# Performance work log

Hardware: AMD Instinct MI355X
Metric: run time of the kernel (lower is better)

Reference implementation:

```python
import jax, jax.numpy as jnp
import numpy as np

GAMMA = 1.4
N_PTS, N_IC, HID = 32768, 16384, 128


def _mlp(layers, p):
    # tanh MLP; layers = list of (W, b), last layer linear
    h = p
    for W, b in layers[:-1]:
        h = jnp.tanh(h @ W + b)
    W, b = layers[-1]
    return h @ W + b


def setup_inputs() -> dict:
    key = jax.random.key(0)
    ks = jax.random.split(key, 16)
    d = {
        "x_train": jax.random.uniform(ks[0], (N_PTS, 3), jnp.float32),
        "x_initial": jax.random.uniform(ks[1], (N_IC, 3), jnp.float32),
        "ic": jax.random.uniform(ks[2], (4, 4), jnp.float32),
    }
    def lin(k, fi, fo):
        return jax.random.normal(k, (fi, fo), jnp.float32) * np.float32(np.sqrt(1.0 / fi))
    dims_m = [(3, HID), (HID, HID), (HID, HID), (HID, 4)]
    dims_n = [(3, HID), (HID, HID), (HID, HID), (HID, 1)]
    for i, (fi, fo) in enumerate(dims_m):
        d[f"mw{i}"] = lin(ks[3 + i], fi, fo)
        d[f"mb{i}"] = jnp.zeros((fo,), jnp.float32)
    for i, (fi, fo) in enumerate(dims_n):
        d[f"nw{i}"] = lin(ks[8 + i], fi, fo)
        d[f"nb{i}"] = jnp.zeros((fo,), jnp.float32)
    return d


def _loss(x_train, x_initial, ic,
          mw0, mb0, mw1, mb1, mw2, mb2, mw3, mb3,
          nw0, nb0, nw1, nb1, nw2, nb2, nw3, nb3):
    layers_m = [(mw0, mb0), (mw1, mb1), (mw2, mb2), (mw3, mb3)]
    layers_n = [(nw0, nb0), (nw1, nb1), (nw2, nb2), (nw3, nb3)]

    def prim(p):  # p: (3,) = (x, y, t)
        o = _mlp(layers_m, p)
        rho, pr, u, v = o[0], o[1], o[2], o[3]
        E = pr / (GAMMA - 1.0) + 0.5 * rho * (u * u + v * v)
        return rho, pr, u, v, E

    def Ufn(p):  # conserved state U1..U4
        rho, pr, u, v, E = prim(p)
        return jnp.stack([rho, rho * u, rho * v, E])

    def quant(p):  # [U1..U4, f1..f4, g1..g4]
        rho, pr, u, v, E = prim(p)
        U = jnp.stack([rho, rho * u, rho * v, E])
        f = jnp.stack([rho * u, rho * u * u + pr, rho * u * v, u * (E + pr)])
        g = jnp.stack([rho * v, rho * u * v, rho * v * v + pr, v * (E + pr)])
        return jnp.concatenate([U, f, g])

    # one fused forward-mode Jacobian sweep replaces 20 torch autograd.grad calls
    J = jax.vmap(jax.jacfwd(quant))(x_train)            # (N, 12, 3)
    Hs = jax.vmap(jax.jacfwd(jax.jacfwd(Ufn)))(x_train)  # (N, 4, 3, 3)

    mu = 0.01 * jnp.squeeze(_mlp(layers_n, x_train), -1) ** 2  # (N,)
    lap = Hs[:, :, 0, 0] + Hs[:, :, 1, 1]               # U_xx + U_yy, (N, 4)
    # res_i = U_i_t + f_i_x + g_i_y - mu * (U_i_xx + U_i_yy)
    res = J[:, 0:4, 2] + J[:, 4:8, 0] + J[:, 8:12, 1] - mu[:, None] * lap
    r = jnp.mean(res ** 2, axis=0)                      # (4,) -> r1..r4

    # initial-condition quadrant loss (masked means, jit-safe)
    pred = _mlp(layers_m, x_initial)                    # (Ni, 4)
    xl = x_initial[:, 0] < 0.5
    xr = x_initial[:, 0] > 0.5
    yt = x_initial[:, 1] > 0.5
    yb = x_initial[:, 1] < 0.5
    perm = jnp.array([0, 3, 1, 2])  # ic columns -> [rho, p, u, v] target order
    init_loss = jnp.float32(0.0)
    for row, mask in ((1, xl & yt), (3, xr & yt), (0, xl & yb), (2, xr & yb)):
        tgt = ic[row][perm]                             # (4,)
        m = mask.astype(pred.dtype)
        denom = jnp.maximum(jnp.sum(m), 1.0)
        init_loss = init_loss + jnp.sum(m[:, None] * (pred - tgt) ** 2) / denom

    return jnp.sum(r) + 10.0 * init_loss + 0.1 * jnp.mean(mu ** 2)


def reference(x_train, x_initial, ic,
              mw0, mb0, mw1, mb1, mw2, mb2, mw3, mb3,
              nw0, nb0, nw1, nb1, nw2, nb2, nw3, nb3):
    return _loss(x_train, x_initial, ic,
                 mw0, mb0, mw1, mb1, mw2, mb2, mw3, mb3,
                 nw0, nb0, nw1, nb1, nw2, nb2, nw3, nb3)
```

## Files before the change

kernel.cpp:

```cpp
#include <hip/hip_runtime.h>

#define NPTS 32768
#define NIC  16384
#define GRID 512
#define BLK  256
#define NW   4

typedef __attribute__((ext_vector_type(8))) _Float16 f16x8;
typedef __attribute__((ext_vector_type(4))) float f32x4;

#define SWZ(e, r) ((e) ^ (((r) & 7) << 3))
#define MFMA16 __builtin_amdgcn_mfma_f32_16x16x32_f16

__device__ __forceinline__ float tanh_fast(float x) {
    float e = __expf(2.0f * x);
    return 1.0f - 2.0f / (e + 1.0f);
}

__device__ __forceinline__ float wave_allsum(float v) {
#pragma unroll
    for (int off = 32; off > 0; off >>= 1) v += __shfl_xor(v, off, 64);
    return v;
}

__device__ __forceinline__ unsigned short f2hb(float x) {
    return __builtin_bit_cast(unsigned short, (_Float16)x);
}
__device__ __forceinline__ uint2 pack4h(float a, float b, float c, float d) {
    return make_uint2((unsigned)f2hb(a) | ((unsigned)f2hb(b) << 16),
                      (unsigned)f2hb(c) | ((unsigned)f2hb(d) << 16));
}

__global__ __launch_bounds__(512) void k_prep(
    const float* __restrict__ mw1, const float* __restrict__ mw2,
    const float* __restrict__ nw1, const float* __restrict__ nw2,
    const float* __restrict__ mw3,
    unsigned short* __restrict__ wt1, unsigned short* __restrict__ wt2,
    unsigned short* __restrict__ nt1, unsigned short* __restrict__ nt2,
    unsigned short* __restrict__ w3t) {
    const int tid = threadIdx.x;
    const int bk = blockIdx.x;
    if (bk == 4) {
        for (int i = tid; i < 2048; i += 512) w3t[i] = 0;
        __syncthreads();
        if (tid < 512) {
            const int j = tid & 127, k = tid >> 7;
            w3t[k * 128 + SWZ(j, k)] = f2hb(mw3[j * 4 + k]);
        }
        return;
    }
    const float* src = (bk == 0) ? mw1 : (bk == 1) ? mw2 : (bk == 2) ? nw1 : nw2;
    unsigned short* dst = (bk == 0) ? wt1 : (bk == 1) ? wt2 : (bk == 2) ? nt1 : nt2;
    __shared__ float sM[128 * 129];
#pragma unroll
    for (int k = 0; k < 32; k++) {
        const int idx = tid + k * 512;
        const int j = idx >> 7, n = idx & 127;
        sM[n * 129 + j] = src[idx];
    }
    __syncthreads();
#pragma unroll
    for (int k = 0; k < 32; k++) {
        const int d = tid + k * 512;
        const int n = d >> 7, js = d & 127;
        const int j = js ^ ((n & 7) << 3);
        dst[d] = f2hb(sM[n * 129 + j]);
    }
}

template <int PT>
__device__ __forceinline__ void hidden_val(const f16x8 (&aW)[2][4], _Float16* sHv,
                                           const float* bias, int wv, int g, int l15) {
    f32x4 acc[2][PT];
#pragma unroll
    for (int rr = 0; rr < 2; rr++)
#pragma unroll
        for (int pt = 0; pt < PT; pt++) acc[rr][pt] = (f32x4){0.f, 0.f, 0.f, 0.f};
#pragma unroll
    for (int ks = 0; ks < 4; ks++) {
        const int ee = SWZ(ks * 32 + g * 8, l15);
#pragma unroll
        for (int pt = 0; pt < PT; pt++) {
            const f16x8 Bv = *(const f16x8*)&sHv[(pt * 16 + l15) * 128 + ee];
            acc[0][pt] = MFMA16(aW[0][ks], Bv, acc[0][pt], 0, 0, 0);
            acc[1][pt] = MFMA16(aW[1][ks], Bv, acc[1][pt], 0, 0, 0);
        }
    }
    __syncthreads();
    float hv[2][PT][4];
#pragma unroll
    for (int rr = 0; rr < 2; rr++)
#pragma unroll
        for (int pt = 0; pt < PT; pt++)
#pragma unroll
            for (int r = 0; r < 4; r++) {
                const int n = wv * 32 + rr * 16 + g * 4 + r;
                hv[rr][pt][r] = tanh_fast(acc[rr][pt][r] + bias[n]);
            }
#pragma unroll
    for (int rr = 0; rr < 2; rr++)
#pragma unroll
        for (int pt = 0; pt < PT; pt++) {
            const int row = pt * 16 + l15;
            *(uint2*)&sHv[row * 128 + SWZ(wv * 32 + rr * 16 + g * 4, row)] =
                pack4h(hv[rr][pt][0], hv[rr][pt][1], hv[rr][pt][2], hv[rr][pt][3]);
        }
}

__device__ __forceinline__ void hidden_res(const f16x8 (&aW)[2][4], _Float16* sH6,
                                           const float* bias, int wv, int g, int l15) {
    f32x4 acc[2][6];
#pragma unroll
    for (int rr = 0; rr < 2; rr++)
#pragma unroll
        for (int c = 0; c < 6; c++) acc[rr][c] = (f32x4){0.f, 0.f, 0.f, 0.f};
#pragma unroll
    for (int ks = 0; ks < 4; ks++) {
        const int ee = SWZ(ks * 32 + g * 8, l15);
#pragma unroll
        for (int c = 0; c < 6; c++) {
            const f16x8 Bv = *(const f16x8*)&sH6[c * 2048 + l15 * 128 + ee];
            acc[0][c] = MFMA16(aW[0][ks], Bv, acc[0][c], 0, 0, 0);
            acc[1][c] = MFMA16(aW[1][ks], Bv, acc[1][c], 0, 0, 0);
        }
    }
    __syncthreads();
    float ch[2][6][4];
#pragma unroll
    for (int rr = 0; rr < 2; rr++)
#pragma unroll
        for (int r = 0; r < 4; r++) {
            const int n = wv * 32 + rr * 16 + g * 4 + r;
            const float z0 = acc[rr][0][r] + bias[n];
            const float a = tanh_fast(z0);
            const float s = 1.f - a * a;
            const float zx = acc[rr][1][r], zy = acc[rr][2][r];
            ch[rr][0][r] = a;
            ch[rr][1][r] = s * zx;
            ch[rr][2][r] = s * zy;
            ch[rr][3][r] = s * acc[rr][3][r];
            ch[rr][4][r] = s * acc[rr][4][r] - 2.f * a * s * zx * zx;
            ch[rr][5][r] = s * acc[rr][5][r] - 2.f * a * s * zy * zy;
        }
#pragma unroll
    for (int rr = 0; rr < 2; rr++) {
        const int eo = l15 * 128 + SWZ(wv * 32 + rr * 16 + g * 4, l15);
#pragma unroll
        for (int c = 0; c < 6; c++)
            *(uint2*)&sH6[c * 2048 + eo] =
                pack4h(ch[rr][c][0], ch[rr][c][1], ch[rr][c][2], ch[rr][c][3]);
    }
}

__global__ __launch_bounds__(BLK) void k_fused(
    const float* __restrict__ xtr, const float* __restrict__ xin,
    const float* __restrict__ icg,
    const float* __restrict__ mw0, const float* __restrict__ mb0,
    const float* __restrict__ mb1, const float* __restrict__ mb2,
    const float* __restrict__ mb3,
    const float* __restrict__ nw0, const float* __restrict__ nb0,
    const float* __restrict__ nb1, const float* __restrict__ nb2,
    const float* __restrict__ nw3, const float* __restrict__ nb3,
    const unsigned short* __restrict__ wt1, const unsigned short* __restrict__ wt2,
    const unsigned short* __restrict__ nt1, const unsigned short* __restrict__ nt2,
    const unsigned short* __restrict__ w3t,
    float* __restrict__ resPart, float* __restrict__ muPart,
    float* __restrict__ icPart) {
    __shared__ __align__(16) _Float16 sH[6 * 2048];
    __shared__ __align__(16) _Float16 sA[2048];
    __shared__ __align__(16) float sO[384];
    __shared__ float sB[520];
    __shared__ float sMu[64];
    __shared__ float sTq[16];
    __shared__ float sRed[NW][8];

    const int tid = threadIdx.x;
    const int lane = tid & 63, wv = tid >> 6;
    const int g = lane >> 4, l15 = lane & 15;
    const int p16 = tid & 15, chunk = tid >> 4;

    f16x8 aW[2][2][4];
    const int arow0 = (wv * 32 + l15) * 128;
    const int arow1 = (wv * 32 + 16 + l15) * 128;
    {
#pragma unroll
        for (int ks = 0; ks < 4; ks++) {
            const int ee = SWZ(ks * 32 + g * 8, l15);
            aW[0][0][ks] = *(const f16x8*)&nt1[arow0 + ee];
            aW[0][1][ks] = *(const f16x8*)&nt1[arow1 + ee];
            aW[1][0][ks] = *(const f16x8*)&nt2[arow0 + ee];
            aW[1][1][ks] = *(const f16x8*)&nt2[arow1 + ee];
        }
    }

    if (tid < 128) { sB[tid] = mb1[tid]; sB[260 + tid] = nb1[tid]; }
    else           { sB[tid] = mb2[tid - 128]; sB[260 + tid] = nb2[tid - 128]; }
    if (tid < 4) sB[256 + tid] = mb3[tid];
    if (tid == 4) sB[516] = nb3[0];
    if (tid < 16) {
        const int k = tid & 3, q = tid >> 2;
        const int row = (q == 0) ? 1 : ((q == 1) ? 3 : ((q == 2) ? 0 : 2));
        const int pc = (k == 0) ? 0 : ((k == 1) ? 3 : ((k == 2) ? 1 : 2));
        sTq[q * 4 + k] = icg[row * 4 + pc];
    }
    for (int i = tid; i < 2048; i += BLK) sA[i] = (_Float16)0.f;
    if (tid < 128) sA[tid] = (_Float16)nw3[tid];

    float wxr[8], wyr[8], wzr[8], wbr[8];
#pragma unroll
    for (int j = 0; j < 8; j++) {
        const int n = chunk * 8 + j;
        wxr[j] = nw0[n]; wyr[j] = nw0[128 + n]; wzr[j] = nw0[256 + n]; wbr[j] = nb0[n];
    }

    float accMu2 = 0.f;
    {
        const int pt0 = blockIdx.x * 64;
        const int ee0 = SWZ(chunk * 8, p16);
#pragma unroll
        for (int pp = 0; pp < 4; pp++) {
            const int p = pt0 + pp * 16 + p16;
            const float x = xtr[p * 3 + 0], y = xtr[p * 3 + 1], t = xtr[p * 3 + 2];
            float hv[8];
#pragma unroll
            for (int j = 0; j < 8; j++)
                hv[j] = tanh_fast(fmaf(wxr[j], x, fmaf(wyr[j], y, fmaf(wzr[j], t, wbr[j]))));
            const uint2 lo = pack4h(hv[0], hv[1], hv[2], hv[3]);
            const uint2 hi = pack4h(hv[4], hv[5], hv[6], hv[7]);
            *(uint4*)&sH[(pp * 16 + p16) * 128 + ee0] = make_uint4(lo.x, lo.y, hi.x, hi.y);
        }
        __syncthreads();
        hidden_val<4>(aW[0], sH, &sB[260], wv, g, l15);
        __syncthreads();
        hidden_val<4>(aW[1], sH, &sB[388], wv, g, l15);
        __syncthreads();
        {
            f32x4 a4 = (f32x4){0.f, 0.f, 0.f, 0.f};
#pragma unroll
            for (int ks = 0; ks < 4; ks++) {
                const int ee = SWZ(ks * 32 + g * 8, l15);
                const f16x8 Af = *(const f16x8*)&sA[l15 * 128 + ee];
                const f16x8 Bv = *(const f16x8*)&sH[(wv * 16 + l15) * 128 + ee];
                a4 = MFMA16(Af, Bv, a4, 0, 0, 0);
            }
            if (g == 0) {
                const float o = a4[0] + sB[516];
                const float muv = 0.01f * o * o;
                sMu[wv * 16 + l15] = muv;
                accMu2 += muv * muv;
            }
        }
        __syncthreads();
    }
    accMu2 = wave_allsum(accMu2);
    if (lane == 0) sRed[wv][0] = accMu2;
    __syncthreads();
    if (tid == 0)
        muPart[blockIdx.x] = sRed[0][0] + sRed[1][0] + sRed[2][0] + sRed[3][0];

#pragma unroll
    for (int j = 0; j < 8; j++) {
        const int n = chunk * 8 + j;
        wxr[j] = mw0[n]; wyr[j] = mw0[128 + n]; wzr[j] = mw0[256 + n]; wbr[j] = mb0[n];
    }
#pragma unroll
    for (int ks = 0; ks < 4; ks++) {
        const int ee = SWZ(ks * 32 + g * 8, l15);
        aW[0][0][ks] = *(const f16x8*)&wt1[arow0 + ee];
        aW[0][1][ks] = *(const f16x8*)&wt1[arow1 + ee];
        aW[1][0][ks] = *(const f16x8*)&wt2[arow0 + ee];
        aW[1][1][ks] = *(const f16x8*)&wt2[arow1 + ee];
    }
    ((uint4*)sA)[tid] = ((const uint4*)w3t)[tid];

    {
        const int pt0 = blockIdx.x * 32;
        const int ee0 = SWZ(chunk * 8, p16);
#pragma unroll
        for (int pp = 0; pp < 2; pp++) {
            const int p = pt0 + pp * 16 + p16;
            const float x = xin[p * 3 + 0], y = xin[p * 3 + 1], t = xin[p * 3 + 2];
            float hv[8];
#pragma unroll
            for (int j = 0; j < 8; j++)
                hv[j] = tanh_fast(fmaf(wxr[j], x, fmaf(wyr[j], y, fmaf(wzr[j], t, wbr[j]))));
            const uint2 lo = pack4h(hv[0], hv[1], hv[2], hv[3]);
            const uint2 hi = pack4h(hv[4], hv[5], hv[6], hv[7]);
            *(uint4*)&sH[(pp * 16 + p16) * 128 + ee0] = make_uint4(lo.x, lo.y, hi.x, hi.y);
        }
        __syncthreads();
        hidden_val<2>(aW[0], sH, &sB[0], wv, g, l15);
        __syncthreads();
        hidden_val<2>(aW[1], sH, &sB[128], wv, g, l15);
        __syncthreads();
        float qs[4] = {0, 0, 0, 0}, qc[4] = {0, 0, 0, 0};
        if (wv < 2) {
            f32x4 a4 = (f32x4){0.f, 0.f, 0.f, 0.f};
#pragma unroll
            for (int ks = 0; ks < 4; ks++) {
                const int ee = SWZ(ks * 32 + g * 8, l15);
                const f16x8 Af = *(const f16x8*)&sA[l15 * 128 + ee];
                const f16x8 Bv = *(const f16x8*)&sH[(wv * 16 + l15) * 128 + ee];
                a4 = MFMA16(Af, Bv, a4, 0, 0, 0);
            }
            if (g == 0) {
                const int p = pt0 + wv * 16 + l15;
                const float o0 = a4[0] + sB[256];
                const float o1 = a4[1] + sB[257];
                const float o2 = a4[2] + sB[258];
                const float o3 = a4[3] + sB[259];
                const float x = xin[p * 3 + 0];
                const float y = xin[p * 3 + 1];
                int quad = -1;
                if (x < 0.5f && y > 0.5f) quad = 0;
                else if (x > 0.5f && y > 0.5f) quad = 1;
                else if (x < 0.5f && y < 0.5f) quad = 2;
                else if (x > 0.5f && y < 0.5f) quad = 3;
                if (quad >= 0) {
                    const float d0 = o0 - sTq[quad * 4 + 0];
                    const float d1 = o1 - sTq[quad * 4 + 1];
                    const float d2 = o2 - sTq[quad * 4 + 2];
                    const float d3 = o3 - sTq[quad * 4 + 3];
                    const float ss = d0 * d0 + d1 * d1 + d2 * d2 + d3 * d3;
#pragma unroll
                    for (int qq = 0; qq < 4; qq++) {
                        qs[qq] += (quad == qq) ? ss : 0.f;
                        qc[qq] += (quad == qq) ? 1.f : 0.f;
                    }
                }
            }
        }
        __syncthreads();
#pragma unroll
        for (int qq = 0; qq < 4; qq++) {
            qs[qq] = wave_allsum(qs[qq]);
            qc[qq] = wave_allsum(qc[qq]);
        }
        if (lane == 0) {
#pragma unroll
            for (int qq = 0; qq < 4; qq++) { sRed[wv][qq] = qs[qq]; sRed[wv][4 + qq] = qc[qq]; }
        }
        __syncthreads();
        if (tid == 0) {
#pragma unroll
            for (int q = 0; q < 8; q++)
                icPart[blockIdx.x * 8 + q] =
                    sRed[0][q] + sRed[1][q] + sRed[2][q] + sRed[3][q];
        }
        __syncthreads();
    }

    float racc0 = 0.f, racc1 = 0.f, racc2 = 0.f, racc3 = 0.f;
    const int base = blockIdx.x * 64;
    for (int b = 0; b < 4; b++) {
        const int pt0 = base + b * 16;
        {
            const int p = pt0 + p16;
            const float x = xtr[p * 3 + 0], y = xtr[p * 3 + 1], t = xtr[p * 3 + 2];
            float ch[6][8];
#pragma unroll
            for (int j = 0; j < 8; j++) {
                const float z = fmaf(wxr[j], x, fmaf(wyr[j], y, fmaf(wzr[j], t, wbr[j])));
                const float a = tanh_fast(z);
                const float s = 1.f - a * a;
                ch[0][j] = a;
                ch[1][j] = s * wxr[j];
                ch[2][j] = s * wyr[j];
                ch[3][j] = s * wzr[j];
                ch[4][j] = -2.f * a * s * wxr[j] * wxr[j];
                ch[5][j] = -2.f * a * s * wyr[j] * wyr[j];
            }
            const int off = p16 * 128 + SWZ(chunk * 8, p16);
#pragma unroll
            for (int c = 0; c < 6; c++) {
                const uint2 lo = pack4h(ch[c][0], ch[c][1], ch[c][2], ch[c][3]);
                const uint2 hi = pack4h(ch[c][4], ch[c][5], ch[c][6], ch[c][7]);
                *(uint4*)&sH[c * 2048 + off] = make_uint4(lo.x, lo.y, hi.x, hi.y);
            }
        }
        __syncthreads();
        hidden_res(aW[0], sH, &sB[0], wv, g, l15);
        __syncthreads();
        hidden_res(aW[1], sH, &sB[128], wv, g, l15);
        __syncthreads();
#pragma unroll
        for (int tt = 0; tt < 2; tt++) {
            const int c = wv + tt * 4;
            if (c < 6) {
                f32x4 a4 = (f32x4){0.f, 0.f, 0.f, 0.f};
#pragma unroll
                for (int ks = 0; ks < 4; ks++) {
                    const int ee = SWZ(ks * 32 + g * 8, l15);
                    const f16x8 Af = *(const f16x8*)&sA[l15 * 128 + ee];
                    const f16x8 Bf = *(const f16x8*)&sH[c * 2048 + l15 * 128 + ee];
                    a4 = MFMA16(Af, Bf, a4, 0, 0, 0);
                }
                if (g == 0) {
                    float4 o = make_float4(a4[0], a4[1], a4[2], a4[3]);
                    if (c == 0) { o.x += sB[256]; o.y += sB[257]; o.z += sB[258]; o.w += sB[259]; }
                    *(float4*)&sO[(c * 16 + l15) * 4] = o;
                }
            }
        }
        __syncthreads();
        if (wv == 0) {
            const int pp = lane & 15;
            const float m = sMu[b * 16 + pp];
            float oq[4][6];
#pragma unroll
            for (int c = 0; c < 6; c++) {
                const float4 o = *(const float4*)&sO[(c * 16 + pp) * 4];
                oq[0][c] = o.x; oq[1][c] = o.y; oq[2][c] = o.z; oq[3][c] = o.w;
            }
            const float rho = oq[0][0], rho_x = oq[0][1], rho_y = oq[0][2],
                        rho_t = oq[0][3], rho_xx = oq[0][4], rho_yy = oq[0][5];
            const float pr = oq[1][0], pr_x = oq[1][1], pr_y = oq[1][2],
                        pr_t = oq[1][3], pr_xx = oq[1][4], pr_yy = oq[1][5];
            const float u = oq[2][0], u_x = oq[2][1], u_y = oq[2][2],
                        u_t = oq[2][3], u_xx = oq[2][4], u_yy = oq[2][5];
            const float v = oq[3][0], v_x = oq[3][1], v_y = oq[3][2],
                        v_t = oq[3][3], v_xx = oq[3][4], v_yy = oq[3][5];

            const float ig1 = 2.5f;
            const float ke = 0.5f * (u * u + v * v);
            const float E = pr * ig1 + rho * ke;
            const float d_x = u * u_x + v * v_x;
            const float d_y = u * u_y + v * v_y;
            const float d_t = u * u_t + v * v_t;
            const float E_x = pr_x * ig1 + rho_x * ke + rho * d_x;
            const float E_y = pr_y * ig1 + rho_y * ke + rho * d_y;
            const float E_t = pr_t * ig1 + rho_t * ke + rho * d_t;
            const float E_xx = pr_xx * ig1 + rho_xx * ke + 2.f * rho_x * d_x +
                               rho * (u_x * u_x + u * u_xx + v_x * v_x + v * v_xx);
            const float E_yy = pr_yy * ig1 + rho_yy * ke + 2.f * rho_y * d_y +
                               rho * (u_y * u_y + u * u_yy + v_y * v_y + v * v_yy);

            const float r1 = rho_t + (rho_x * u + rho * u_x) + (rho_y * v + rho * v_y)
                           - m * (rho_xx + rho_yy);
            const float r2 = (rho_t * u + rho * u_t)
                           + (rho_x * u * u + 2.f * rho * u * u_x + pr_x)
                           + (rho_y * u * v + rho * u_y * v + rho * u * v_y)
                           - m * ((rho_xx * u + 2.f * rho_x * u_x + rho * u_xx)
                                + (rho_yy * u + 2.f * rho_y * u_y + rho * u_yy));
            const float r3 = (rho_t * v + rho * v_t)
                           + (rho_x * u * v + rho * u_x * v + rho * u * v_x)
                           + (rho_y * v * v + 2.f * rho * v * v_y + pr_y)
                           - m * ((rho_xx * v + 2.f * rho_x * v_x + rho * v_xx)
                                + (rho_yy * v + 2.f * rho_y * v_y + rho * v_yy));
            const float r4 = E_t
                           + (u_x * (E + pr) + u * (E_x + pr_x))
                           + (v_y * (E + pr) + v * (E_y + pr_y))
                           - m * (E_xx + E_yy);
            if (lane < 16) {
                racc0 += r1 * r1; racc1 += r2 * r2;
                racc2 += r3 * r3; racc3 += r4 * r4;
            }
        }
        __syncthreads();
    }

    if (wv == 0) {
        racc0 = wave_allsum(racc0);
        racc1 = wave_allsum(racc1);
        racc2 = wave_allsum(racc2);
        racc3 = wave_allsum(racc3);
        if (lane == 0) {
            resPart[blockIdx.x * 4 + 0] = racc0;
            resPart[blockIdx.x * 4 + 1] = racc1;
            resPart[blockIdx.x * 4 + 2] = racc2;
            resPart[blockIdx.x * 4 + 3] = racc3;
        }
    }
}

__global__ void k_fin(const float* __restrict__ resPart, const float* __restrict__ muPart,
                      const float* __restrict__ icPart, float* __restrict__ out) {
    const int lane = threadIdx.x;
    float r[4] = {0, 0, 0, 0};
    float m2 = 0.f;
    float qs[4] = {0, 0, 0, 0}, qc[4] = {0, 0, 0, 0};
    for (int b = lane; b < GRID; b += 64) {
#pragma unroll
        for (int i = 0; i < 4; i++) r[i] += resPart[b * 4 + i];
        m2 += muPart[b];
#pragma unroll
        for (int q = 0; q < 4; q++) {
            qs[q] += icPart[b * 8 + q];
            qc[q] += icPart[b * 8 + 4 + q];
        }
    }
#pragma unroll
    for (int i = 0; i < 4; i++) r[i] = wave_allsum(r[i]);
    m2 = wave_allsum(m2);
#pragma unroll
    for (int q = 0; q < 4; q++) { qs[q] = wave_allsum(qs[q]); qc[q] = wave_allsum(qc[q]); }
    if (lane == 0) {
        const float sumr = (r[0] + r[1] + r[2] + r[3]) / (float)NPTS;
        float init_loss = 0.f;
#pragma unroll
        for (int q = 0; q < 4; q++) init_loss += qs[q] / fmaxf(qc[q], 1.f);
        out[0] = sumr + 10.f * init_loss + 0.1f * (m2 / (float)NPTS);
    }
}

extern "C" void kernel_launch(void* const* d_in, const int* in_sizes, int n_in,
                              void* d_out, int out_size, void* d_ws, size_t ws_size,
                              hipStream_t stream) {
    const float* xtr = (const float*)d_in[0];
    const float* xin = (const float*)d_in[1];
    const float* icg = (const float*)d_in[2];
    const float* mw0 = (const float*)d_in[3];
    const float* mb0 = (const float*)d_in[4];
    const float* mw1 = (const float*)d_in[5];
    const float* mb1 = (const float*)d_in[6];
    const float* mw2 = (const float*)d_in[7];
    const float* mb2 = (const float*)d_in[8];
    const float* mw3 = (const float*)d_in[9];
    const float* mb3 = (const float*)d_in[10];
    const float* nw0 = (const float*)d_in[11];
    const float* nb0 = (const float*)d_in[12];
    const float* nw1 = (const float*)d_in[13];
    const float* nb1 = (const float*)d_in[14];
    const float* nw2 = (const float*)d_in[15];
    const float* nb2 = (const float*)d_in[16];
    const float* nw3 = (const float*)d_in[17];
    const float* nb3 = (const float*)d_in[18];

    float* wsf = (float*)d_ws;
    float* resPart = wsf;
    float* muPart = wsf + 2048;
    float* icPart = wsf + 2560;
    unsigned short* wt1 = (unsigned short*)(wsf + 6656);
    unsigned short* wt2 = wt1 + 16384;
    unsigned short* nt1 = wt2 + 16384;
    unsigned short* nt2 = nt1 + 16384;
    unsigned short* w3t = nt2 + 16384;

    k_prep<<<5, 512, 0, stream>>>(mw1, mw2, nw1, nw2, mw3, wt1, wt2, nt1, nt2, w3t);
    k_fused<<<GRID, BLK, 0, stream>>>(xtr, xin, icg,
                                      mw0, mb0, mb1, mb2, mb3,
                                      nw0, nb0, nb1, nb2, nw3, nb3,
                                      wt1, wt2, nt1, nt2, w3t,
                                      resPart, muPart, icPart);
    k_fin<<<1, 64, 0, stream>>>(resPart, muPart, icPart, (float*)d_out);
}
```

Baseline: 71.02 us.

## Double grid size and cut register pressure to raise occupancy

Doubles the grid so each block handles half as many points, which halves the per-block tile loops. The weight fragments for the two hidden layers now share a single register array that is reloaded between layers, and the first-layer weights move from per-thread registers into shared memory, with launch bounds requesting 4 blocks per CU. The aim is more resident waves on each CU so latency is hidden better. In exchange, weight fragments are re-read from global or L2 memory for every tile, and the per-block partial buffers and workspace offsets grow.

```diff
diff --git a/kernel.cpp b/kernel.cpp
--- a/kernel.cpp
+++ b/kernel.cpp
@@ -2,7 +2,7 @@
 
 #define NPTS 32768
 #define NIC  16384
-#define GRID 512
+#define GRID 1024
 #define BLK  256
 #define NW   4
 
@@ -65,6 +65,17 @@
         const int n = d >> 7, js = d & 127;
         const int j = js ^ ((n & 7) << 3);
         dst[d] = f2hb(sM[n * 129 + j]);
+    }
+}
+
+__device__ __forceinline__ void load_aw(f16x8 (&aW)[2][4],
+                                        const unsigned short* __restrict__ w,
+                                        int arow0, int arow1, int g, int l15) {
+#pragma unroll
+    for (int ks = 0; ks < 4; ks++) {
+        const int ee = SWZ(ks * 32 + g * 8, l15);
+        aW[0][ks] = *(const f16x8*)&w[arow0 + ee];
+        aW[1][ks] = *(const f16x8*)&w[arow1 + ee];
     }
 }
 
@@ -152,7 +163,7 @@
     }
 }
 
-__global__ __launch_bounds__(BLK) void k_fused(
+__global__ __launch_bounds__(BLK, 4) void k_fused(
     const float* __restrict__ xtr, const float* __restrict__ xin,
     const float* __restrict__ icg,
     const float* __restrict__ mw0, const float* __restrict__ mb0,
@@ -168,9 +179,10 @@
     float* __restrict__ icPart) {
     __shared__ __align__(16) _Float16 sH[6 * 2048];
     __shared__ __align__(16) _Float16 sA[2048];
+    __shared__ __align__(16) float sW0[2][512];
     __shared__ __align__(16) float sO[384];
     __shared__ float sB[520];
-    __shared__ float sMu[64];
+    __shared__ float sMu[32];
     __shared__ float sTq[16];
     __shared__ float sRed[NW][8];
 
@@ -178,20 +190,11 @@
     const int lane = tid & 63, wv = tid >> 6;
     const int g = lane >> 4, l15 = lane & 15;
     const int p16 = tid & 15, chunk = tid >> 4;
-
-    f16x8 aW[2][2][4];
     const int arow0 = (wv * 32 + l15) * 128;
     const int arow1 = (wv * 32 + 16 + l15) * 128;
-    {
-#pragma unroll
-        for (int ks = 0; ks < 4; ks++) {
-            const int ee = SWZ(ks * 32 + g * 8, l15);
-            aW[0][0][ks] = *(const f16x8*)&nt1[arow0 + ee];
-            aW[0][1][ks] = *(const f16x8*)&nt1[arow1 + ee];
-            aW[1][0][ks] = *(const f16x8*)&nt2[arow0 + ee];
-            aW[1][1][ks] = *(const f16x8*)&nt2[arow1 + ee];
-        }
-    }
+
+    f16x8 aW[2][4];
+    load_aw(aW, nt1, arow0, arow1, g, l15);
 
     if (tid < 128) { sB[tid] = mb1[tid]; sB[260 + tid] = nb1[tid]; }
     else           { sB[tid] = mb2[tid - 128]; sB[260 + tid] = nb2[tid - 128]; }
@@ -203,38 +206,41 @@
         const int pc = (k == 0) ? 0 : ((k == 1) ? 3 : ((k == 2) ? 1 : 2));
         sTq[q * 4 + k] = icg[row * 4 + pc];
     }
+    for (int i = tid; i < 512; i += BLK) {
+        sW0[0][i] = (i < 384) ? nw0[i] : nb0[i - 384];
+        sW0[1][i] = (i < 384) ? mw0[i] : mb0[i - 384];
+    }
     for (int i = tid; i < 2048; i += BLK) sA[i] = (_Float16)0.f;
     if (tid < 128) sA[tid] = (_Float16)nw3[tid];
-
-    float wxr[8], wyr[8], wzr[8], wbr[8];
-#pragma unroll
-    for (int j = 0; j < 8; j++) {
-        const int n = chunk * 8 + j;
-        wxr[j] = nw0[n]; wyr[j] = nw0[128 + n]; wzr[j] = nw0[256 + n]; wbr[j] = nb0[n];
-    }
+    __syncthreads();
 
     float accMu2 = 0.f;
     {
-        const int pt0 = blockIdx.x * 64;
+        const int pt0 = blockIdx.x * 32;
         const int ee0 = SWZ(chunk * 8, p16);
-#pragma unroll
-        for (int pp = 0; pp < 4; pp++) {
+        const float* w0 = &sW0[0][0];
+#pragma unroll
+        for (int pp = 0; pp < 2; pp++) {
             const int p = pt0 + pp * 16 + p16;
             const float x = xtr[p * 3 + 0], y = xtr[p * 3 + 1], t = xtr[p * 3 + 2];
             float hv[8];
 #pragma unroll
-            for (int j = 0; j < 8; j++)
-                hv[j] = tanh_fast(fmaf(wxr[j], x, fmaf(wyr[j], y, fmaf(wzr[j], t, wbr[j]))));
+            for (int j = 0; j < 8; j++) {
+                const int n = chunk * 8 + j;
+                hv[j] = tanh_fast(fmaf(w0[n], x, fmaf(w0[128 + n], y,
+                                       fmaf(w0[256 + n], t, w0[384 + n]))));
+            }
             const uint2 lo = pack4h(hv[0], hv[1], hv[2], hv[3]);
             const uint2 hi = pack4h(hv[4], hv[5], hv[6], hv[7]);
             *(uint4*)&sH[(pp * 16 + p16) * 128 + ee0] = make_uint4(lo.x, lo.y, hi.x, hi.y);
         }
         __syncthreads();
-        hidden_val<4>(aW[0], sH, &sB[260], wv, g, l15);
-        __syncthreads();
-        hidden_val<4>(aW[1], sH, &sB[388], wv, g, l15);
-        __syncthreads();
-        {
+        hidden_val<2>(aW, sH, &sB[260], wv, g, l15);
+        load_aw(aW, nt2, arow0, arow1, g, l15);
+        __syncthreads();
+        hidden_val<2>(aW, sH, &sB[388], wv, g, l15);
+        __syncthreads();
+        if (wv < 2) {
             f32x4 a4 = (f32x4){0.f, 0.f, 0.f, 0.f};
 #pragma unroll
             for (int ks = 0; ks < 4; ks++) {
@@ -258,53 +264,45 @@
     if (tid == 0)
         muPart[blockIdx.x] = sRed[0][0] + sRed[1][0] + sRed[2][0] + sRed[3][0];
 
-#pragma unroll
-    for (int j = 0; j < 8; j++) {
-        const int n = chunk * 8 + j;
-        wxr[j] = mw0[n]; wyr[j] = mw0[128 + n]; wzr[j] = mw0[256 + n]; wbr[j] = mb0[n];
-    }
-#pragma unroll
-    for (int ks = 0; ks < 4; ks++) {
-        const int ee = SWZ(ks * 32 + g * 8, l15);
-        aW[0][0][ks] = *(const f16x8*)&wt1[arow0 + ee];
-        aW[0][1][ks] = *(const f16x8*)&wt1[arow1 + ee];
-        aW[1][0][ks] = *(const f16x8*)&wt2[arow0 + ee];
-        aW[1][1][ks] = *(const f16x8*)&wt2[arow1 + ee];
-    }
     ((uint4*)sA)[tid] = ((const uint4*)w3t)[tid];
+    load_aw(aW, wt1, arow0, arow1, g, l15);
 
     {
-        const int pt0 = blockIdx.x * 32;
+        const int pt0 = blockIdx.x * 16;
         const int ee0 = SWZ(chunk * 8, p16);
-#pragma unroll
-        for (int pp = 0; pp < 2; pp++) {
-            const int p = pt0 + pp * 16 + p16;
+        const float* w0 = &sW0[1][0];
+        {
+            const int p = pt0 + p16;
             const float x = xin[p * 3 + 0], y = xin[p * 3 + 1], t = xin[p * 3 + 2];
             float hv[8];
 #pragma unroll
-            for (int j = 0; j < 8; j++)
-                hv[j] = tanh_fast(fmaf(wxr[j], x, fmaf(wyr[j], y, fmaf(wzr[j], t, wbr[j]))));
+            for (int j = 0; j < 8; j++) {
+                const int n = chunk * 8 + j;
+                hv[j] = tanh_fast(fmaf(w0[n], x, fmaf(w0[128 + n], y,
+                                       fmaf(w0[256 + n], t, w0[384 + n]))));
+            }
             const uint2 lo = pack4h(hv[0], hv[1], hv[2], hv[3]);
             const uint2 hi = pack4h(hv[4], hv[5], hv[6], hv[7]);
-            *(uint4*)&sH[(pp * 16 + p16) * 128 + ee0] = make_uint4(lo.x, lo.y, hi.x, hi.y);
-        }
-        __syncthreads();
-        hidden_val<2>(aW[0], sH, &sB[0], wv, g, l15);
-        __syncthreads();
-        hidden_val<2>(aW[1], sH, &sB[128], wv, g, l15);
+            *(uint4*)&sH[p16 * 128 + ee0] = make_uint4(lo.x, lo.y, hi.x, hi.y);
+        }
+        __syncthreads();
+        hidden_val<1>(aW, sH, &sB[0], wv, g, l15);
+        load_aw(aW, wt2, arow0, arow1, g, l15);
+        __syncthreads();
+        hidden_val<1>(aW, sH, &sB[128], wv, g, l15);
         __syncthreads();
         float qs[4] = {0, 0, 0, 0}, qc[4] = {0, 0, 0, 0};
-        if (wv < 2) {
+        if (wv == 0) {
             f32x4 a4 = (f32x4){0.f, 0.f, 0.f, 0.f};
 #pragma unroll
             for (int ks = 0; ks < 4; ks++) {
                 const int ee = SWZ(ks * 32 + g * 8, l15);
                 const f16x8 Af = *(const f16x8*)&sA[l15 * 128 + ee];
-                const f16x8 Bv = *(const f16x8*)&sH[(wv * 16 + l15) * 128 + ee];
+                const f16x8 Bv = *(const f16x8*)&sH[l15 * 128 + ee];
                 a4 = MFMA16(Af, Bv, a4, 0, 0, 0);
             }
             if (g == 0) {
-                const int p = pt0 + wv * 16 + l15;
+                const int p = pt0 + l15;
                 const float o0 = a4[0] + sB[256];
                 const float o1 = a4[1] + sB[257];
                 const float o2 = a4[2] + sB[258];
@@ -351,24 +349,28 @@
     }
 
     float racc0 = 0.f, racc1 = 0.f, racc2 = 0.f, racc3 = 0.f;
-    const int base = blockIdx.x * 64;
-    for (int b = 0; b < 4; b++) {
+    const int base = blockIdx.x * 32;
+    for (int b = 0; b < 2; b++) {
         const int pt0 = base + b * 16;
+        load_aw(aW, wt1, arow0, arow1, g, l15);
         {
             const int p = pt0 + p16;
             const float x = xtr[p * 3 + 0], y = xtr[p * 3 + 1], t = xtr[p * 3 + 2];
+            const float* w0 = &sW0[1][0];
             float ch[6][8];
 #pragma unroll
             for (int j = 0; j < 8; j++) {
-                const float z = fmaf(wxr[j], x, fmaf(wyr[j], y, fmaf(wzr[j], t, wbr[j])));
+                const int n = chunk * 8 + j;
+                const float wx = w0[n], wy = w0[128 + n], wz = w0[256 + n];
+                const float z = fmaf(wx, x, fmaf(wy, y, fmaf(wz, t, w0[384 + n])));
                 const float a = tanh_fast(z);
                 const float s = 1.f - a * a;
                 ch[0][j] = a;
-                ch[1][j] = s * wxr[j];
-                ch[2][j] = s * wyr[j];
-                ch[3][j] = s * wzr[j];
-                ch[4][j] = -2.f * a * s * wxr[j] * wxr[j];
-                ch[5][j] = -2.f * a * s * wyr[j] * wyr[j];
+                ch[1][j] = s * wx;
+                ch[2][j] = s * wy;
+                ch[3][j] = s * wz;
+                ch[4][j] = -2.f * a * s * wx * wx;
+                ch[5][j] = -2.f * a * s * wy * wy;
             }
             const int off = p16 * 128 + SWZ(chunk * 8, p16);
 #pragma unroll
@@ -379,9 +381,10 @@
             }
         }
         __syncthreads();
-        hidden_res(aW[0], sH, &sB[0], wv, g, l15);
-        __syncthreads();
-        hidden_res(aW[1], sH, &sB[128], wv, g, l15);
+        hidden_res(aW, sH, &sB[0], wv, g, l15);
+        load_aw(aW, wt2, arow0, arow1, g, l15);
+        __syncthreads();
+        hidden_res(aW, sH, &sB[128], wv, g, l15);
         __syncthreads();
 #pragma unroll
         for (int tt = 0; tt < 2; tt++) {
@@ -528,9 +531,9 @@
 
     float* wsf = (float*)d_ws;
     float* resPart = wsf;
-    float* muPart = wsf + 2048;
-    float* icPart = wsf + 2560;
-    unsigned short* wt1 = (unsigned short*)(wsf + 6656);
+    float* muPart = wsf + 4096;
+    float* icPart = wsf + 5120;
+    unsigned short* wt1 = (unsigned short*)(wsf + 13312);
     unsigned short* wt2 = wt1 + 16384;
     unsigned short* nt1 = wt2 + 16384;
     unsigned short* nt2 = nt1 + 16384;
```

New measurement: 70.54 us. No clear change (-0.7%).
